# Kernel optimization log

Measured on AMD Instinct MI355X. Metric: run time of the kernel, lower is better.

## Reference

```python
import jax, jax.numpy as jnp
import numpy as np

EPS = 1e-5        # BatchNorm1d default eps
SLOPE = 0.01      # torch LeakyReLU default negative slope


def setup_inputs() -> dict:
    key = jax.random.key(0)
    ks = jax.random.split(key, 10)
    N3, N2, N1, N0 = 4096, 16384, 65536, 262144  # coarse -> fine point hierarchy
    return {
        "feats": jax.random.normal(ks[0], (N3, 258), jnp.float32),
        "skip1": jax.random.normal(ks[1], (N0, 128), jnp.float32),
        "skip2": jax.random.normal(ks[2], (N1, 256), jnp.float32),
        "skip3": jax.random.normal(ks[3], (N2, 512), jnp.float32),
        "idx1": jax.random.randint(ks[4], (N2,), 0, N3, jnp.int32),
        "idx2": jax.random.randint(ks[5], (N1,), 0, N2, jnp.int32),
        "idx3": jax.random.randint(ks[6], (N0,), 0, N1, jnp.int32),
        "W1": jax.random.normal(ks[7], (770, 129), jnp.float32) * 0.05,
        "b1": jnp.zeros((129,), jnp.float32),
        "g1": jnp.ones((129,), jnp.float32),
        "be1": jnp.zeros((129,), jnp.float32),
        "W2": jax.random.normal(ks[8], (385, 64), jnp.float32) * 0.05,
        "b2": jnp.zeros((64,), jnp.float32),
        "g2": jnp.ones((64,), jnp.float32),
        "be2": jnp.zeros((64,), jnp.float32),
        "W3": jax.random.normal(ks[9], (192, 34), jnp.float32) * 0.05,
        "b3": jnp.zeros((34,), jnp.float32),
    }


def _bn(y, g, b):
    # training-mode batch norm over the points dimension (biased variance)
    m = y.mean(axis=0)
    v = y.var(axis=0)
    return (y - m) * jax.lax.rsqrt(v + EPS) * g + b


def _lrelu(x):
    return jnp.where(x >= 0, x, SLOPE * x)


def reference(feats, skip1, skip2, skip3, idx1, idx2, idx3,
              W1, b1, g1, be1, W2, b2, g2, be2, W3, b3):
    # stage 1: nearest upsample N3->N2, concat skip3, conv1x1 + BN + LeakyReLU
    x = jnp.concatenate([feats[idx1], skip3], axis=1)        # [N2, 770]
    x = _lrelu(_bn(x @ W1 + b1, g1, be1))                    # [N2, 129]
    # stage 2: upsample N2->N1
    x = jnp.concatenate([x[idx2], skip2], axis=1)            # [N1, 385]
    x = _lrelu(_bn(x @ W2 + b2, g2, be2))                    # [N1, 64]
    # stage 3: upsample N1->N0, plain conv1x1 (no BN / no activation)
    x = jnp.concatenate([x[idx3], skip1], axis=1)            # [N0, 192]
    return x @ W3 + b3                                       # [N0, 34]
```

## Files before the change

### kernel.cpp

```cpp
#include <hip/hip_runtime.h>

#define EPS 1e-5f
#define SLOPE 0.01f

typedef __attribute__((ext_vector_type(4))) float f32x4;
typedef __attribute__((ext_vector_type(8))) short bf16x8;

__device__ __forceinline__ short f2bf(float f) {
    unsigned u = __float_as_uint(f);
    unsigned r = (u + 0x7FFFu + ((u >> 16) & 1u)) >> 16;
    return (short)r;
}
__device__ __forceinline__ float lrelu(float v) { return v >= 0.f ? v : SLOPE * v; }

__device__ __forceinline__ void gload16(const float* g, float* l) {
    __builtin_amdgcn_global_load_lds(
        (const __attribute__((address_space(1))) unsigned*)g,
        (__attribute__((address_space(3))) unsigned*)l, 16, 0, 0);
}
__device__ __forceinline__ void gload4(const float* g, float* l) {
    __builtin_amdgcn_global_load_lds(
        (const __attribute__((address_space(1))) unsigned*)g,
        (__attribute__((address_space(3))) unsigned*)l, 4, 0, 0);
}

#define WCASE(N) case N: asm volatile("s_waitcnt vmcnt(" #N ")" ::: "memory"); break;
__device__ __forceinline__ void wait_vm(int n) {
    switch (n) {
    WCASE(0) WCASE(1) WCASE(2) WCASE(3) WCASE(4) WCASE(5) WCASE(6) WCASE(7)
    WCASE(8) WCASE(9) WCASE(10) WCASE(11) WCASE(12) WCASE(13) WCASE(14) WCASE(15)
    WCASE(16) WCASE(17) WCASE(18) WCASE(19) WCASE(20) WCASE(21) WCASE(22) WCASE(23)
    WCASE(24) WCASE(25) WCASE(26) WCASE(27) WCASE(28) WCASE(29) WCASE(30) WCASE(31)
    WCASE(32) WCASE(33) WCASE(34) WCASE(35) WCASE(36) WCASE(37) WCASE(38) WCASE(39)
    WCASE(40) WCASE(41) WCASE(42) WCASE(43) WCASE(44) WCASE(45) WCASE(46) WCASE(47)
    WCASE(48) WCASE(49) WCASE(50) WCASE(51) WCASE(52) WCASE(53) WCASE(54) WCASE(55)
    WCASE(56) WCASE(57) WCASE(58) WCASE(59) WCASE(60) WCASE(61) WCASE(62) WCASE(63)
    default: asm volatile("s_waitcnt vmcnt(0)" ::: "memory"); break;
    }
}

__device__ __forceinline__ int swz_cf(int s, int r) {
    return ((((s >> 1) ^ r) & 7) << 1) | (s & 1);
}

__global__ void prep(const float* __restrict__ W1, const float* __restrict__ W2,
                     const float* __restrict__ W3,
                     short* __restrict__ Wt1, short* __restrict__ Wt2,
                     short* __restrict__ Wt3, float* __restrict__ stats,
                     float* __restrict__ y1)
{
    const int id0 = blockIdx.x * 256 + threadIdx.x;
    const int str = gridDim.x * 256;
    for (int id = id0; id < 2048; id += str) stats[id] = 0.f;
    for (int id = id0; id < 26 * 9 * 512; id += str) {
        int e = id & 7, lane = (id >> 3) & 63, g = id >> 9;
        int t = g / 9, nt = g - t * 9;
        int kv = t * 32 + (lane >> 4) * 8 + e;
        int n  = nt * 16 + (lane & 15);
        float v = 0.f; int ks = -1;
        if (kv < 258) ks = kv; else if (kv >= 320) ks = kv - 62;
        if (ks >= 0 && ks < 770 && n < 129) v = W1[ks * 129 + n];
        Wt1[id] = f2bf(v);
    }
    for (int id = id0; id < 14 * 4 * 512; id += str) {
        int e = id & 7, lane = (id >> 3) & 63, g = id >> 9;
        int t = g >> 2, nt = g & 3;
        int kv = t * 32 + (lane >> 4) * 8 + e;
        int n  = nt * 16 + (lane & 15);
        float v = 0.f; int ks = -1;
        if (kv < 129) ks = kv; else if (kv >= 192) ks = kv - 63;
        if (ks >= 0 && ks < 385) v = W2[ks * 64 + n];
        Wt2[id] = f2bf(v);
    }
    for (int id = id0; id < 6 * 3 * 512; id += str) {
        int e = id & 7, lane = (id >> 3) & 63, g = id >> 9;
        int t = g / 3, nt = g - t * 3;
        int kv = t * 32 + (lane >> 4) * 8 + e;
        int n  = nt * 16 + (lane & 15);
        float v = (n < 34) ? W3[kv * 34 + n] : 0.f;
        Wt3[id] = f2bf(v);
    }
    for (int id = id0; id < 16384 * 64; id += str) {
        int r = id >> 6, c = id & 63;
        y1[(size_t)r * 192 + 128 + c] = 0.f;
    }
}

template<int XD, int SD, int NCX, int NCS, int NT, int NVALID, int OD,
         bool XA16, int XCLAMP, int BNC, bool STATS, int BMODE, int MINW>
__global__ __launch_bounds__(256, MINW)
void mfma_stage(const float* __restrict__ xsrc, const float* __restrict__ skip,
                const int* __restrict__ idx, const short* __restrict__ Wt,
                const float* __restrict__ bias,
                const float* __restrict__ bnsum, const float* __restrict__ bnsq,
                const float* __restrict__ bng, const float* __restrict__ bnbe,
                float invN, float* __restrict__ out,
                float* __restrict__ ssum, float* __restrict__ ssq)
{
    constexpr int NC = NCX + NCS;
    constexpr bool BN = (BNC > 0);
    constexpr int NPAD = NT * 16;

    __shared__ __align__(16) float abuf[4][3][1024];
    __shared__ __align__(16) float bnl[BN ? 2 * NCX * 64 : 4];

    const int tid  = threadIdx.x;
    const int wave = tid >> 6, lane = tid & 63;
    const int lr = lane & 15;
    const int kg = lane >> 4;
    const int row0w = (blockIdx.x * 4 + wave) * 16;
    const short* wtf = Wt + (lane << 3);
    float* awave = &abuf[wave][0][0];

    if (BN) {
        for (int i = tid; i < NCX * 64; i += 256) {
            float sc = 0.f, sh = 0.f;
            if (i < BNC) {
                float m   = bnsum[i] * invN;
                float var = fmaf(-m, m, bnsq[i] * invN);
                float rs  = rsqrtf(var + EPS);
                sc = rs * bng[i];
                sh = fmaf(-m, sc, bnbe[i]);
            }
            bnl[i] = sc;
            bnl[NCX * 64 + i] = sh;
        }
        __syncthreads();
    }

    const float* prow[XA16 ? 4 : 16];
    if constexpr (XA16) {
#pragma unroll
        for (int q = 0; q < 4; ++q)
            prow[q] = xsrc + (size_t)idx[row0w + q * 4 + kg] * XD;
    } else {
#pragma unroll
        for (int j = 0; j < 16; ++j)
            prow[j] = xsrc + (size_t)idx[row0w + j] * XD;
    }

    auto sD = [](int c) -> int {
        if (c < 0 || c >= NC) return 0;
        return (c < NCX && !XA16) ? 16 : 4;
    };
    auto sB = [](int c) -> int {
        if (c < 0 || c >= NC) return 0;
        return 2 * NT;
    };

    auto issue = [&](int c) {
        float* wb = awave + (c % 3) * 1024;
        if (c < NCX) {
            if constexpr (XA16) {
#pragma unroll
                for (int q = 0; q < 4; ++q) {
                    const int rl = q * 4 + kg;
                    const int cf = swz_cf(lane & 15, rl);
                    gload16(prow[q] + c * 64 + cf * 4, wb + q * 256);
                }
            } else {
#pragma unroll
                for (int j = 0; j < 16; ++j) {
                    const int cf = swz_cf(lane >> 2, j);
                    int col = c * 64 + cf * 4 + (lane & 3);
                    if (XCLAMP > 0 && c == NCX - 1) col = min(col, XCLAMP - 1);
                    gload4(prow[j] + col, wb + j * 64);
                }
            }
        } else {
            const int jc = c - NCX;
#pragma unroll
            for (int q = 0; q < 4; ++q) {
                const int rl = q * 4 + kg;
                const int cf = swz_cf(lane & 15, rl);
                gload16(skip + (size_t)(row0w + rl) * SD + jc * 64 + cf * 4,
                        wb + q * 256);
            }
        }
    };

    bf16x8 Bp[(BMODE == 2) ? 2 * NC * NT : 1];
    bf16x8 Bf[(BMODE == 1) ? 3 : 1][2][NT];
    auto loadB = [&](int cc) {
#pragma unroll
        for (int tt = 0; tt < 2; ++tt)
#pragma unroll
            for (int nt = 0; nt < NT; ++nt)
                Bf[cc % 3][tt][nt] =
                    *(const bf16x8*)(wtf + (((2 * cc + tt) * NT + nt) << 9));
    };

    f32x4 acc[NT];
#pragma unroll
    for (int nt = 0; nt < NT; ++nt) acc[nt] = (f32x4){0.f, 0.f, 0.f, 0.f};

    if constexpr (BMODE == 2) {
#pragma unroll
        for (int tv = 0; tv < 2 * NC; ++tv)
#pragma unroll
            for (int nt = 0; nt < NT; ++nt)
                Bp[tv * NT + nt] = *(const bf16x8*)(wtf + ((tv * NT + nt) << 9));
    }

    issue(0);
    if constexpr (BMODE == 1) loadB(0);
    if (NC > 1) issue(1);
    if constexpr (BMODE == 1) { if (NC > 1) loadB(1); }

#pragma unroll
    for (int c = 0; c < NC; ++c) {
        if (c + 2 < NC) issue(c + 2);
        int w;
        if constexpr (BMODE == 0)      w = sD(c+1) + sD(c+2) + sB(c-1) + sB(c-2);
        else if constexpr (BMODE == 1) w = sD(c+1) + sD(c+2) + sB(c) + sB(c+1);
        else                           w = sD(c+1) + sD(c+2);
        wait_vm(w > 63 ? 63 : w);
        if constexpr (BMODE == 1) { if (c + 2 < NC) loadB(c + 2); }

        const float* wb = awave + (c % 3) * 1024;
#pragma unroll
        for (int tt = 0; tt < 2; ++tt) {
            const int p0 = tt * 4 + kg;
            const float* fp = wb + lr * 64 + ((p0 ^ (lr & 7)) << 3);
            f32x4 lo = *(const f32x4*)fp;
            f32x4 hi = *(const f32x4*)(fp + 4);
            float v[8];
#pragma unroll
            for (int e = 0; e < 4; ++e) { v[e] = lo[e]; v[e + 4] = hi[e]; }
            if (BN && c < NCX) {
                const int kb = c * 64 + tt * 32 + kg * 8;
                f32x4 c0 = *(const f32x4*)&bnl[kb];
                f32x4 c1 = *(const f32x4*)&bnl[kb + 4];
                f32x4 h0 = *(const f32x4*)&bnl[NCX * 64 + kb];
                f32x4 h1 = *(const f32x4*)&bnl[NCX * 64 + kb + 4];
#pragma unroll
                for (int e = 0; e < 4; ++e) {
                    v[e]     = lrelu(fmaf(v[e],     c0[e], h0[e]));
                    v[e + 4] = lrelu(fmaf(v[e + 4], c1[e], h1[e]));
                }
            }
            bf16x8 a;
#pragma unroll
            for (int e = 0; e < 8; ++e) a[e] = f2bf(v[e]);
#pragma unroll
            for (int nt = 0; nt < NT; ++nt) {
                bf16x8 b;
                if constexpr (BMODE == 2)      b = Bp[(2 * c + tt) * NT + nt];
                else if constexpr (BMODE == 1) b = Bf[c % 3][tt][nt];
                else b = *(const bf16x8*)(wtf + (((2 * c + tt) * NT + nt) << 9));
                acc[nt] = __builtin_amdgcn_mfma_f32_16x16x32_bf16(a, b, acc[nt], 0, 0, 0);
            }
        }
    }

#pragma unroll
    for (int nt = 0; nt < NT; ++nt) {
        const int n = nt * 16 + lr;
        const float bv = (n < NVALID) ? bias[n] : 0.f;
#pragma unroll
        for (int r = 0; r < 4; ++r) acc[nt][r] += bv;
        if (n < NVALID) {
#pragma unroll
            for (int r = 0; r < 4; ++r)
                out[(size_t)(row0w + kg * 4 + r) * OD + n] = acc[nt][r];
        }
    }

    if constexpr (STATS) {
        float* ls = &abuf[0][0][0];
        __syncthreads();
        for (int i = tid; i < 2 * NPAD; i += 256) ls[i] = 0.f;
        __syncthreads();
#pragma unroll
        for (int nt = 0; nt < NT; ++nt) {
            float s = acc[nt][0] + acc[nt][1] + acc[nt][2] + acc[nt][3];
            float q = acc[nt][0]*acc[nt][0] + acc[nt][1]*acc[nt][1]
                    + acc[nt][2]*acc[nt][2] + acc[nt][3]*acc[nt][3];
            s += __shfl_xor(s, 16, 64);
            s += __shfl_xor(s, 32, 64);
            q += __shfl_xor(q, 16, 64);
            q += __shfl_xor(q, 32, 64);
            if (lane < 16) {
                atomicAdd(&ls[nt * 16 + lr], s);
                atomicAdd(&ls[NPAD + nt * 16 + lr], q);
            }
        }
        __syncthreads();
        for (int i = tid; i < NPAD; i += 256) {
            atomicAdd(&ssum[i], ls[i]);
            atomicAdd(&ssq[i], ls[NPAD + i]);
        }
    }
}

extern "C" void kernel_launch(void* const* d_in, const int* in_sizes, int n_in,
                              void* d_out, int out_size, void* d_ws, size_t ws_size,
                              hipStream_t stream) {
    const float* feats = (const float*)d_in[0];
    const float* skip1 = (const float*)d_in[1];
    const float* skip2 = (const float*)d_in[2];
    const float* skip3 = (const float*)d_in[3];
    const int*   idx1  = (const int*)d_in[4];
    const int*   idx2  = (const int*)d_in[5];
    const int*   idx3  = (const int*)d_in[6];
    const float* W1    = (const float*)d_in[7];
    const float* b1    = (const float*)d_in[8];
    const float* g1    = (const float*)d_in[9];
    const float* be1   = (const float*)d_in[10];
    const float* W2    = (const float*)d_in[11];
    const float* b2    = (const float*)d_in[12];
    const float* g2    = (const float*)d_in[13];
    const float* be2   = (const float*)d_in[14];
    const float* W3    = (const float*)d_in[15];
    const float* b3    = (const float*)d_in[16];

    float* ws   = (float*)d_ws;
    float* sum1 = ws;        float* sq1 = ws + 256;
    float* sum2 = ws + 512;  float* sq2 = ws + 768;
    short* Wt1  = (short*)(ws + 2048);
    short* Wt2  = Wt1 + 119808;
    short* Wt3  = Wt2 + 28672;
    float* y1   = ws + 80896;
    float* y2   = y1 + 16384 * 192;
    float* outp = (float*)d_out;

    prep<<<512, 256, 0, stream>>>(W1, W2, W3, Wt1, Wt2, Wt3, ws, y1);

    mfma_stage<258, 512, 5, 8, 9, 129, 192, false, 258, 0, true, 0, 2>
        <<<256, 256, 0, stream>>>(feats, skip3, idx1, Wt1, b1,
                                  nullptr, nullptr, nullptr, nullptr, 0.f,
                                  y1, sum1, sq1);

    mfma_stage<192, 256, 3, 4, 4, 64, 64, true, 0, 129, true, 1, 3>
        <<<1024, 256, 0, stream>>>(y1, skip2, idx2, Wt2, b2,
                                   sum1, sq1, g1, be1, 1.f / 16384.f,
                                   y2, sum2, sq2);

    mfma_stage<64, 128, 1, 2, 3, 34, 34, true, 0, 64, false, 2, 3>
        <<<4096, 256, 0, stream>>>(y2, skip1, idx3, Wt3, b3,
                                   sum2, sq2, g2, be2, 1.f / 65536.f,
                                   outp, nullptr, nullptr);
}
```

Measured before the change: 125.3 us.

## Store intermediate activations in bf16 and spread BN stat atomics over partitions

Intermediate activations y1 and y2 are now written as bf16 instead of fp32. This halves the bytes moved by the gathered upsample loads and the intermediate stores, and the gathered rows are loaded into LDS as 16-byte bf16 chunks with an XOR swizzle. BatchNorm sum and sum-of-squares atomics are split across 8 partial buffers keyed by block index, which cuts same-address contention, and the consumer stage adds the partials back together. In exchange, pre-BN values are rounded to bf16 before normalization, which adds rounding error to the BN path.

```diff
diff --git a/kernel.cpp b/kernel.cpp
--- a/kernel.cpp
+++ b/kernel.cpp
@@ -11,14 +11,17 @@
     unsigned r = (u + 0x7FFFu + ((u >> 16) & 1u)) >> 16;
     return (short)r;
 }
+__device__ __forceinline__ float bf2f(short h) {
+    return __uint_as_float(((unsigned)(unsigned short)h) << 16);
+}
 __device__ __forceinline__ float lrelu(float v) { return v >= 0.f ? v : SLOPE * v; }
 
-__device__ __forceinline__ void gload16(const float* g, float* l) {
+__device__ __forceinline__ void gload16(const void* g, float* l) {
     __builtin_amdgcn_global_load_lds(
         (const __attribute__((address_space(1))) unsigned*)g,
         (__attribute__((address_space(3))) unsigned*)l, 16, 0, 0);
 }
-__device__ __forceinline__ void gload4(const float* g, float* l) {
+__device__ __forceinline__ void gload4(const void* g, float* l) {
     __builtin_amdgcn_global_load_lds(
         (const __attribute__((address_space(1))) unsigned*)g,
         (__attribute__((address_space(3))) unsigned*)l, 4, 0, 0);
@@ -47,54 +50,53 @@
                      const float* __restrict__ W3,
                      short* __restrict__ Wt1, short* __restrict__ Wt2,
                      short* __restrict__ Wt3, float* __restrict__ stats,
-                     float* __restrict__ y1)
+                     short* __restrict__ y1h)
 {
     const int id0 = blockIdx.x * 256 + threadIdx.x;
     const int str = gridDim.x * 256;
-    for (int id = id0; id < 2048; id += str) stats[id] = 0.f;
+    for (int id = id0; id < 4096; id += str) stats[id] = 0.f;
     for (int id = id0; id < 26 * 9 * 512; id += str) {
-        int e = id & 7, lane = (id >> 3) & 63, g = id >> 9;
+        int e = id & 7, ln = (id >> 3) & 63, g = id >> 9;
         int t = g / 9, nt = g - t * 9;
-        int kv = t * 32 + (lane >> 4) * 8 + e;
-        int n  = nt * 16 + (lane & 15);
+        int kv = t * 32 + (ln >> 4) * 8 + e;
+        int n  = nt * 16 + (ln & 15);
         float v = 0.f; int ks = -1;
         if (kv < 258) ks = kv; else if (kv >= 320) ks = kv - 62;
         if (ks >= 0 && ks < 770 && n < 129) v = W1[ks * 129 + n];
         Wt1[id] = f2bf(v);
     }
     for (int id = id0; id < 14 * 4 * 512; id += str) {
-        int e = id & 7, lane = (id >> 3) & 63, g = id >> 9;
+        int e = id & 7, ln = (id >> 3) & 63, g = id >> 9;
         int t = g >> 2, nt = g & 3;
-        int kv = t * 32 + (lane >> 4) * 8 + e;
-        int n  = nt * 16 + (lane & 15);
+        int kv = t * 32 + (ln >> 4) * 8 + e;
+        int n  = nt * 16 + (ln & 15);
         float v = 0.f; int ks = -1;
         if (kv < 129) ks = kv; else if (kv >= 192) ks = kv - 63;
         if (ks >= 0 && ks < 385) v = W2[ks * 64 + n];
         Wt2[id] = f2bf(v);
     }
     for (int id = id0; id < 6 * 3 * 512; id += str) {
-        int e = id & 7, lane = (id >> 3) & 63, g = id >> 9;
+        int e = id & 7, ln = (id >> 3) & 63, g = id >> 9;
         int t = g / 3, nt = g - t * 3;
-        int kv = t * 32 + (lane >> 4) * 8 + e;
-        int n  = nt * 16 + (lane & 15);
+        int kv = t * 32 + (ln >> 4) * 8 + e;
+        int n  = nt * 16 + (ln & 15);
         float v = (n < 34) ? W3[kv * 34 + n] : 0.f;
         Wt3[id] = f2bf(v);
     }
-    for (int id = id0; id < 16384 * 64; id += str) {
-        int r = id >> 6, c = id & 63;
-        y1[(size_t)r * 192 + 128 + c] = 0.f;
-    }
-}
-
-template<int XD, int SD, int NCX, int NCS, int NT, int NVALID, int OD,
-         bool XA16, int XCLAMP, int BNC, bool STATS, int BMODE, int MINW>
+    for (int id = id0; id < 16384 * 64; id += str)
+        y1h[(size_t)(id >> 6) * 192 + 128 + (id & 63)] = 0;
+}
+
+template<int XD, int SD, int NCX, int NCS, int NT, int NVALID, int ODe,
+         int XMODE, int XCLAMP, int BNC, int BNSTR, bool STATS, int BMODE, int MINW,
+         bool OUTBF>
 __global__ __launch_bounds__(256, MINW)
-void mfma_stage(const float* __restrict__ xsrc, const float* __restrict__ skip,
+void mfma_stage(const void* __restrict__ xsrcv, const float* __restrict__ skip,
                 const int* __restrict__ idx, const short* __restrict__ Wt,
                 const float* __restrict__ bias,
                 const float* __restrict__ bnsum, const float* __restrict__ bnsq,
                 const float* __restrict__ bng, const float* __restrict__ bnbe,
-                float invN, float* __restrict__ out,
+                float invN, void* __restrict__ outv,
                 float* __restrict__ ssum, float* __restrict__ ssq)
 {
     constexpr int NC = NCX + NCS;
@@ -116,8 +118,14 @@
         for (int i = tid; i < NCX * 64; i += 256) {
             float sc = 0.f, sh = 0.f;
             if (i < BNC) {
-                float m   = bnsum[i] * invN;
-                float var = fmaf(-m, m, bnsq[i] * invN);
+                float s = 0.f, q = 0.f;
+#pragma unroll
+                for (int p = 0; p < 8; ++p) {
+                    s += bnsum[p * BNSTR + i];
+                    q += bnsq[p * BNSTR + i];
+                }
+                float m   = s * invN;
+                float var = fmaf(-m, m, q * invN);
                 float rs  = rsqrtf(var + EPS);
                 sc = rs * bng[i];
                 sh = fmaf(-m, sc, bnbe[i]);
@@ -128,20 +136,23 @@
         __syncthreads();
     }
 
-    const float* prow[XA16 ? 4 : 16];
-    if constexpr (XA16) {
-#pragma unroll
-        for (int q = 0; q < 4; ++q)
-            prow[q] = xsrc + (size_t)idx[row0w + q * 4 + kg] * XD;
+    const float* prowf[XMODE == 0 ? 16 : 1];
+    const short* prowh[XMODE == 2 ? 2 : 1];
+    if constexpr (XMODE == 0) {
+#pragma unroll
+        for (int j = 0; j < 16; ++j)
+            prowf[j] = (const float*)xsrcv + (size_t)idx[row0w + j] * XD;
     } else {
 #pragma unroll
-        for (int j = 0; j < 16; ++j)
-            prow[j] = xsrc + (size_t)idx[row0w + j] * XD;
+        for (int i = 0; i < 2; ++i)
+            prowh[i] = (const short*)xsrcv
+                       + (size_t)idx[row0w + i * 8 + (lane >> 3)] * XD;
     }
 
     auto sD = [](int c) -> int {
         if (c < 0 || c >= NC) return 0;
-        return (c < NCX && !XA16) ? 16 : 4;
+        if (c < NCX) return (XMODE == 0) ? 16 : 2;
+        return 4;
     };
     auto sB = [](int c) -> int {
         if (c < 0 || c >= NC) return 0;
@@ -151,12 +162,12 @@
     auto issue = [&](int c) {
         float* wb = awave + (c % 3) * 1024;
         if (c < NCX) {
-            if constexpr (XA16) {
-#pragma unroll
-                for (int q = 0; q < 4; ++q) {
-                    const int rl = q * 4 + kg;
-                    const int cf = swz_cf(lane & 15, rl);
-                    gload16(prow[q] + c * 64 + cf * 4, wb + q * 256);
+            if constexpr (XMODE == 2) {
+#pragma unroll
+                for (int i = 0; i < 2; ++i) {
+                    const int r  = i * 8 + (lane >> 3);
+                    const int ss = (lane & 7) ^ (r & 7);
+                    gload16(prowh[i] + c * 64 + ss * 8, wb + i * 256);
                 }
             } else {
 #pragma unroll
@@ -164,7 +175,7 @@
                     const int cf = swz_cf(lane >> 2, j);
                     int col = c * 64 + cf * 4 + (lane & 3);
                     if (XCLAMP > 0 && c == NCX - 1) col = min(col, XCLAMP - 1);
-                    gload4(prow[j] + col, wb + j * 64);
+                    gload4(prowf[j] + col, wb + j * 64);
                 }
             }
         } else {
@@ -220,28 +231,36 @@
         const float* wb = awave + (c % 3) * 1024;
 #pragma unroll
         for (int tt = 0; tt < 2; ++tt) {
-            const int p0 = tt * 4 + kg;
-            const float* fp = wb + lr * 64 + ((p0 ^ (lr & 7)) << 3);
-            f32x4 lo = *(const f32x4*)fp;
-            f32x4 hi = *(const f32x4*)(fp + 4);
-            float v[8];
-#pragma unroll
-            for (int e = 0; e < 4; ++e) { v[e] = lo[e]; v[e + 4] = hi[e]; }
-            if (BN && c < NCX) {
-                const int kb = c * 64 + tt * 32 + kg * 8;
-                f32x4 c0 = *(const f32x4*)&bnl[kb];
-                f32x4 c1 = *(const f32x4*)&bnl[kb + 4];
-                f32x4 h0 = *(const f32x4*)&bnl[NCX * 64 + kb];
-                f32x4 h1 = *(const f32x4*)&bnl[NCX * 64 + kb + 4];
-#pragma unroll
-                for (int e = 0; e < 4; ++e) {
-                    v[e]     = lrelu(fmaf(v[e],     c0[e], h0[e]));
-                    v[e + 4] = lrelu(fmaf(v[e + 4], c1[e], h1[e]));
+            bf16x8 a;
+            if (c < NCX && XMODE == 2) {
+                const short* hp = (const short*)wb + lr * 64
+                                  + (((tt * 4 + kg) ^ (lr & 7)) << 3);
+                bf16x8 ar = *(const bf16x8*)hp;
+                if (BN) {
+                    const int kb = c * 64 + tt * 32 + kg * 8;
+                    f32x4 c0 = *(const f32x4*)&bnl[kb];
+                    f32x4 c1 = *(const f32x4*)&bnl[kb + 4];
+                    f32x4 h0 = *(const f32x4*)&bnl[NCX * 64 + kb];
+                    f32x4 h1 = *(const f32x4*)&bnl[NCX * 64 + kb + 4];
+#pragma unroll
+                    for (int e = 0; e < 4; ++e) {
+                        a[e]     = f2bf(lrelu(fmaf(bf2f(ar[e]),     c0[e], h0[e])));
+                        a[e + 4] = f2bf(lrelu(fmaf(bf2f(ar[e + 4]), c1[e], h1[e])));
+                    }
+                } else {
+                    a = ar;
                 }
-            }
-            bf16x8 a;
-#pragma unroll
-            for (int e = 0; e < 8; ++e) a[e] = f2bf(v[e]);
+            } else {
+                const int p0 = tt * 4 + kg;
+                const float* fp = wb + lr * 64 + ((p0 ^ (lr & 7)) << 3);
+                f32x4 lo = *(const f32x4*)fp;
+                f32x4 hi = *(const f32x4*)(fp + 4);
+                float v[8];
+#pragma unroll
+                for (int e = 0; e < 4; ++e) { v[e] = lo[e]; v[e + 4] = hi[e]; }
+#pragma unroll
+                for (int e = 0; e < 8; ++e) a[e] = f2bf(v[e]);
+            }
 #pragma unroll
             for (int nt = 0; nt < NT; ++nt) {
                 bf16x8 b;
@@ -261,8 +280,11 @@
         for (int r = 0; r < 4; ++r) acc[nt][r] += bv;
         if (n < NVALID) {
 #pragma unroll
-            for (int r = 0; r < 4; ++r)
-                out[(size_t)(row0w + kg * 4 + r) * OD + n] = acc[nt][r];
+            for (int r = 0; r < 4; ++r) {
+                const size_t o = (size_t)(row0w + kg * 4 + r) * ODe + n;
+                if constexpr (OUTBF) ((short*)outv)[o] = f2bf(acc[nt][r]);
+                else                 ((float*)outv)[o] = acc[nt][r];
+            }
         }
     }
 
@@ -286,9 +308,10 @@
             }
         }
         __syncthreads();
+        const int part = blockIdx.x & 7;
         for (int i = tid; i < NPAD; i += 256) {
-            atomicAdd(&ssum[i], ls[i]);
-            atomicAdd(&ssq[i], ls[NPAD + i]);
+            atomicAdd(&ssum[part * NPAD + i], ls[i]);
+            atomicAdd(&ssq[part * NPAD + i], ls[NPAD + i]);
         }
     }
 }
@@ -315,29 +338,31 @@
     const float* b3    = (const float*)d_in[16];
 
     float* ws   = (float*)d_ws;
-    float* sum1 = ws;        float* sq1 = ws + 256;
-    float* sum2 = ws + 512;  float* sq2 = ws + 768;
-    short* Wt1  = (short*)(ws + 2048);
+    float* sum1 = ws;
+    float* sq1  = ws + 1152;
+    float* sum2 = ws + 2304;
+    float* sq2  = ws + 2816;
+    short* Wt1  = (short*)(ws + 4096);
     short* Wt2  = Wt1 + 119808;
     short* Wt3  = Wt2 + 28672;
-    float* y1   = ws + 80896;
-    float* y2   = y1 + 16384 * 192;
+    short* y1h  = Wt3 + 9216;
+    short* y2h  = y1h + (size_t)16384 * 192;
     float* outp = (float*)d_out;
 
-    prep<<<512, 256, 0, stream>>>(W1, W2, W3, Wt1, Wt2, Wt3, ws, y1);
-
-    mfma_stage<258, 512, 5, 8, 9, 129, 192, false, 258, 0, true, 0, 2>
+    prep<<<512, 256, 0, stream>>>(W1, W2, W3, Wt1, Wt2, Wt3, ws, y1h);
+
+    mfma_stage<258, 512, 5, 8, 9, 129, 192, 0, 258, 0, 1, true, 0, 2, true>
         <<<256, 256, 0, stream>>>(feats, skip3, idx1, Wt1, b1,
                                   nullptr, nullptr, nullptr, nullptr, 0.f,
-                                  y1, sum1, sq1);
-
-    mfma_stage<192, 256, 3, 4, 4, 64, 64, true, 0, 129, true, 1, 3>
-        <<<1024, 256, 0, stream>>>(y1, skip2, idx2, Wt2, b2,
+                                  y1h, sum1, sq1);
+
+    mfma_stage<192, 256, 3, 4, 4, 64, 64, 2, 0, 129, 144, true, 1, 3, true>
+        <<<1024, 256, 0, stream>>>(y1h, skip2, idx2, Wt2, b2,
                                    sum1, sq1, g1, be1, 1.f / 16384.f,
-                                   y2, sum2, sq2);
-
-    mfma_stage<64, 128, 1, 2, 3, 34, 34, true, 0, 64, false, 2, 3>
-        <<<4096, 256, 0, stream>>>(y2, skip1, idx3, Wt3, b3,
+                                   y2h, sum2, sq2);
+
+    mfma_stage<64, 128, 1, 2, 3, 34, 34, 2, 0, 64, 64, false, 2, 3, false>
+        <<<4096, 256, 0, stream>>>(y2h, skip1, idx3, Wt3, b3,
                                    sum2, sq2, g2, be2, 1.f / 65536.f,
                                    outp, nullptr, nullptr);
 }
```

Result: faster. 104.3 us (median of 2 runs) (-16.7%).
